# Kernel optimization log

Hardware: AMD Instinct MI355X
Metric: run time of the kernel (lower is better)

## Reference

```python
import jax, jax.numpy as jnp
import numpy as np

IN_CH = 256
OUT_CH = 256
DIM = 8
HEADS = IN_CH // DIM            # 32
TOTAL = HEADS * DIM             # 256
C3 = 3 * TOTAL                  # 768
SCALES = (3, 5)
EPS = 1e-15


def _conv(x, w, b, groups=1, pad=0):
    # x: [B,C,H,W], w: [O, C//groups, kh, kw]
    y = jax.lax.conv_general_dilated(
        x, w, window_strides=(1, 1), padding=[(pad, pad), (pad, pad)],
        dimension_numbers=("NCHW", "OIHW", "NCHW"), feature_group_count=groups)
    return y + b[None, :, None, None]


def setup_inputs() -> dict:
    key = jax.random.key(0)
    ks = jax.random.split(key, 16)
    s = 0.02
    inp = {
        "x": jax.random.normal(ks[0], (8, IN_CH, 64, 64), jnp.float32),
        "qkv_w": jax.random.normal(ks[1], (C3, IN_CH, 1, 1), jnp.float32) * s,
        "qkv_b": jnp.zeros((C3,), jnp.float32),
        # scale 3: depthwise conv (groups=C3) then 1x1 grouped conv (groups=HEADS)
        "dw3_w": jax.random.normal(ks[2], (C3, 1, 3, 3), jnp.float32) * s,
        "dw3_b": jnp.zeros((C3,), jnp.float32),
        "pw3_w": jax.random.normal(ks[3], (C3, C3 // HEADS, 1, 1), jnp.float32) * s,
        "pw3_b": jnp.zeros((C3,), jnp.float32),
        # scale 5
        "dw5_w": jax.random.normal(ks[4], (C3, 1, 5, 5), jnp.float32) * s,
        "dw5_b": jnp.zeros((C3,), jnp.float32),
        "pw5_w": jax.random.normal(ks[5], (C3, C3 // HEADS, 1, 1), jnp.float32) * s,
        "pw5_b": jnp.zeros((C3,), jnp.float32),
        # proj: in = TOTAL*(1+len(SCALES)) = 768 -> OUT_CH
        "proj_w": jax.random.normal(ks[6], (OUT_CH, TOTAL * (1 + len(SCALES)), 1, 1), jnp.float32) * s,
        "proj_b": jnp.zeros((OUT_CH,), jnp.float32),
    }
    return inp


def _relu_linear_att(qkv):
    B, C, H, W = qkv.shape
    qkv = qkv.reshape(B, -1, 3 * DIM, H * W)          # [B, h, 3d, N]
    q = jax.nn.relu(qkv[:, :, :DIM])                   # [B, h, d, N]
    k = jax.nn.relu(qkv[:, :, DIM:2 * DIM])            # [B, h, d, N]
    v = qkv[:, :, 2 * DIM:]                            # [B, h, d, N]
    v = jnp.concatenate([v, jnp.ones_like(v[:, :, :1])], axis=2)  # pad ones -> [B,h,d+1,N]
    vk = jnp.einsum("bhdn,bhen->bhde", v, k)          # [B, h, d+1, d]
    out = jnp.einsum("bhde,bhen->bhdn", vk, q)        # [B, h, d+1, N]
    out = out[:, :, :-1] / (out[:, :, -1:] + EPS)      # normalize by denominator row
    return out.reshape(B, -1, H, W)


def reference(x, qkv_w, qkv_b, dw3_w, dw3_b, pw3_w, pw3_b,
              dw5_w, dw5_b, pw5_w, pw5_b, proj_w, proj_b):
    qkv = _conv(x, qkv_w, qkv_b)                                   # [B, 768, H, W]
    s3 = _conv(_conv(qkv, dw3_w, dw3_b, groups=C3, pad=1), pw3_w, pw3_b, groups=HEADS)
    s5 = _conv(_conv(qkv, dw5_w, dw5_b, groups=C3, pad=2), pw5_w, pw5_b, groups=HEADS)
    multi = jnp.concatenate([qkv, s3, s5], axis=1)                 # [B, 2304, H, W]
    att = _relu_linear_att(multi)                                  # [B, 768, H, W]
    return _conv(att, proj_w, proj_b)                              # [B, 256, H, W]
```

## Files before the change

kernel.cpp:

```cpp
#include <hip/hip_runtime.h>
#include <hip/hip_bf16.h>

#define C3 768
#define PIX 4096
#define NB 8

typedef __attribute__((ext_vector_type(8))) short bf16x8;
typedef __attribute__((ext_vector_type(4))) float f32x4;

__device__ __forceinline__ unsigned short f2bf(float f) {
    unsigned int u = __float_as_uint(f);
    u += 0x7fffu + ((u >> 16) & 1u);
    return (unsigned short)(u >> 16);
}
__device__ __forceinline__ float bf2f(unsigned short h) {
    return __uint_as_float((unsigned int)h << 16);
}

__device__ __forceinline__ void gload_lds16(const void* g, void* l) {
    __builtin_amdgcn_global_load_lds(
        (const __attribute__((address_space(1))) void*)g,
        (__attribute__((address_space(3))) void*)l, 16, 0, 0);
}

__global__ __launch_bounds__(256) void split3_kernel(
    const float* __restrict__ src, unsigned short* __restrict__ d,
    size_t stride, int n)
{
    int i = blockIdx.x * 256 + threadIdx.x;
    if (i < n) {
        float f = src[i];
        unsigned short h0 = f2bf(f);  float r1 = f - bf2f(h0);
        unsigned short h1 = f2bf(r1); float r2 = r1 - bf2f(h1);
        d[i]              = h0;
        d[i + stride]     = h1;
        d[i + 2 * stride] = f2bf(r2);
    }
}

__global__ __launch_bounds__(256) void split2_kernel(
    const float* __restrict__ src, unsigned short* __restrict__ d,
    size_t stride, int n)
{
    int i = blockIdx.x * 256 + threadIdx.x;
    if (i < n) {
        float f = src[i];
        unsigned short h0 = f2bf(f);
        d[i]          = h0;
        d[i + stride] = f2bf(f - bf2f(h0));
    }
}

__global__ __launch_bounds__(256) void transpose_split3_kernel(
    const float* __restrict__ src, unsigned short* __restrict__ d, size_t stride)
{
    __shared__ float t[32][33];
    const int b  = blockIdx.z;
    const int p0 = blockIdx.x * 32;
    const int k0 = blockIdx.y * 32;
    const int tx = threadIdx.x & 31, ty = threadIdx.x >> 5;

    const float* s = src + ((size_t)b * 256 + k0) * PIX + p0;
#pragma unroll
    for (int i = 0; i < 4; ++i)
        t[ty + i * 8][tx] = s[(size_t)(ty + i * 8) * PIX + tx];
    __syncthreads();
#pragma unroll
    for (int i = 0; i < 4; ++i) {
        const int p = ty + i * 8;
        float f = t[tx][p];
        unsigned short h0 = f2bf(f);  float r1 = f - bf2f(h0);
        unsigned short h1 = f2bf(r1); float r2 = r1 - bf2f(h1);
        size_t o = ((size_t)b * PIX + p0 + p) * 256 + k0 + tx;
        d[o]              = h0;
        d[o + stride]     = h1;
        d[o + 2 * stride] = f2bf(r2);
    }
}

template <int K, int S>
__global__ __launch_bounds__(256) void gemm_mfma_splitS(
    const unsigned short* __restrict__ A, const unsigned short* __restrict__ Bm,
    const float* __restrict__ bias, float* __restrict__ Y,
    int Mtiles, int M, size_t strideA, size_t strideB)
{
    __shared__ char lds[S * 24576];
    char* sA[S];
    char* sB[S];
#pragma unroll
    for (int s = 0; s < S; ++s) {
        sA[s] = lds + s * 16384;
        sB[s] = lds + S * 16384 + s * 8192;
    }

    const int nwg = gridDim.x;
    const int per = nwg >> 3;
    const int bid = blockIdx.x;
    const int wg  = (bid & 7) * per + (bid >> 3);
    const int tm  = wg % Mtiles;
    const int tn  = wg / Mtiles;
    const int bm  = tm * 128;
    const int gn0 = tn * 64;

    const int tid  = threadIdx.x;
    const int lane = tid & 63;
    const int wv   = tid >> 6;
    const int m0w  = (wv & 1) * 64;
    const int n0w  = (wv >> 1) * 32;

    const int l8  = lane >> 3;
    const int c16 = (lane & 7) * 16;
    const int gchunk = (c16 ^ (l8 << 4)) >> 1;
    const unsigned short* gA = A  + (size_t)(bm  + wv * 8 + l8) * K + gchunk;
    const unsigned short* gB = Bm + (size_t)(gn0 + wv * 8 + l8) * K + gchunk;
    const int ldsw = wv * 1024;

    f32x4 acc[4][2] = {};

    for (int k0 = 0; k0 < K; k0 += 64) {
        __syncthreads();
#pragma unroll
        for (int s = 0; s < S; ++s) {
#pragma unroll
            for (int j = 0; j < 4; ++j)
                gload_lds16(gA + s * strideA + (size_t)j * 32 * K + k0,
                            sA[s] + ldsw + j * 4096);
#pragma unroll
            for (int j = 0; j < 2; ++j)
                gload_lds16(gB + s * strideB + (size_t)j * 32 * K + k0,
                            sB[s] + ldsw + j * 4096);
        }
        __syncthreads();

#pragma unroll
        for (int kk = 0; kk < 2; ++kk) {
            const int kbyte = (kk * 32 + (lane >> 4) * 8) * 2;
            bf16x8 bfr[S][2];
#pragma unroll
            for (int ni = 0; ni < 2; ++ni) {
                const int r = n0w + ni * 16 + (lane & 15);
                const int byte = r * 128 + (kbyte ^ ((r & 7) << 4));
#pragma unroll
                for (int s = 0; s < S; ++s)
                    bfr[s][ni] = *(const bf16x8*)(sB[s] + byte);
            }
#pragma unroll
            for (int mi = 0; mi < 4; ++mi) {
                bf16x8 afr[S];
                const int r = m0w + mi * 16 + (lane & 15);
                const int byte = r * 128 + (kbyte ^ ((r & 7) << 4));
#pragma unroll
                for (int s = 0; s < S; ++s)
                    afr[s] = *(const bf16x8*)(sA[s] + byte);
#pragma unroll
                for (int ni = 0; ni < 2; ++ni) {
#pragma unroll
                    for (int i = 0; i < S; ++i)
#pragma unroll
                        for (int j = 0; j < S; ++j)
                            if (i + j < S)
                                acc[mi][ni] = __builtin_amdgcn_mfma_f32_16x16x32_bf16(
                                    afr[i], bfr[j][ni], acc[mi][ni], 0, 0, 0);
                }
            }
        }
    }

    const int b  = gn0 >> 12;
    const int p0 = gn0 & 4095;
#pragma unroll
    for (int mi = 0; mi < 4; ++mi)
#pragma unroll
        for (int ni = 0; ni < 2; ++ni) {
            const int p = p0 + n0w + ni * 16 + (lane & 15);
#pragma unroll
            for (int i = 0; i < 4; ++i) {
                const int m = bm + m0w + mi * 16 + (lane >> 4) * 4 + i;
                Y[((size_t)b * M + m) * PIX + p] = acc[mi][ni][i] + bias[m];
            }
        }
}

__global__ __launch_bounds__(256, 4) void dwpw_kernel(
    const float* __restrict__ qkv,
    const float* __restrict__ w3,  const float* __restrict__ b3,
    const float* __restrict__ w5,  const float* __restrict__ b5,
    const float* __restrict__ pw3w, const float* __restrict__ pw3b,
    const float* __restrict__ pw5w, const float* __restrict__ pw5b,
    float* __restrict__ t3, float* __restrict__ t5)
{
    __shared__ float tile[2][8][68];

    const int g   = blockIdx.y;
    const int b   = blockIdx.z;
    const int tid = threadIdx.x;
    const int p   = blockIdx.x * 256 + tid;
    const int r0  = blockIdx.x * 4;
    const int c0  = g * 24;
    const int lr  = tid >> 6;
    const int lc  = tid & 63;

    const float* src0 = qkv + ((size_t)b * C3 + c0) * PIX;

    float o3[24], o5[24];
#pragma unroll
    for (int co = 0; co < 24; ++co) {
        o3[co] = pw3b[c0 + co];
        o5[co] = pw5b[c0 + co];
    }

    auto stage = [&](int ic, int buf) {
        const float* src = src0 + (size_t)ic * PIX;
#pragma unroll
        for (int j = 0; j < 2; ++j) {
            const int rr = (tid >> 6) + j * 4;
            const int cc = tid & 63;
            const int gr = r0 - 2 + rr, gc = cc - 2;
            float v = 0.f;
            if ((unsigned)gr < 64u && (unsigned)gc < 64u) v = src[gr * 64 + gc];
            tile[buf][rr][cc] = v;
        }
        if (tid < 32) {
            const int rr = tid >> 2;
            const int cc = 64 + (tid & 3);
            const int gr = r0 - 2 + rr, gc = cc - 2;
            float v = 0.f;
            if ((unsigned)gr < 64u && (unsigned)gc < 64u) v = src[gr * 64 + gc];
            tile[buf][rr][cc] = v;
        }
    };

    stage(0, 0);
    for (int ic = 0; ic < 24; ++ic) {
        __syncthreads();
        if (ic + 1 < 24) stage(ic + 1, (ic + 1) & 1);

        const int c = c0 + ic;
        const float* k5 = w5 + c * 25;
        const float* k3 = w3 + c * 9;
        const float (*T)[68] = tile[ic & 1];

        float acc3 = b3[c], acc5 = b5[c];
#pragma unroll
        for (int dy = 0; dy < 5; ++dy) {
#pragma unroll
            for (int dx = 0; dx < 5; ++dx) {
                const float v = T[lr + dy][lc + dx];
                acc5 = fmaf(k5[dy * 5 + dx], v, acc5);
                if (dy >= 1 && dy <= 3 && dx >= 1 && dx <= 3)
                    acc3 = fmaf(k3[(dy - 1) * 3 + (dx - 1)], v, acc3);
            }
        }

        const float* w3g = pw3w + (size_t)c0 * 24 + ic;
        const float* w5g = pw5w + (size_t)c0 * 24 + ic;
#pragma unroll
        for (int co = 0; co < 24; ++co) {
            o3[co] = fmaf(w3g[co * 24], acc3, o3[co]);
            o5[co] = fmaf(w5g[co * 24], acc5, o5[co]);
        }
    }

    float* dst3 = t3 + ((size_t)b * C3 + c0) * PIX + p;
    float* dst5 = t5 + ((size_t)b * C3 + c0) * PIX + p;
#pragma unroll
    for (int co = 0; co < 24; ++co) {
        dst3[(size_t)co * PIX] = o3[co];
        dst5[(size_t)co * PIX] = o5[co];
    }
}

__global__ __launch_bounds__(256) void vk_reduce_kernel(
    const float* __restrict__ qkv, const float* __restrict__ s3,
    const float* __restrict__ s5, float* __restrict__ vkout)
{
    const int hh = blockIdx.x;
    const int b  = blockIdx.y;
    const float* src = (hh < 32) ? qkv : ((hh < 64) ? s3 : s5);
    const int ch0 = (hh & 31) * 24;
    const float* base = src + ((size_t)b * C3 + ch0) * PIX;

    float acc[9][8] = {};
    for (int p = threadIdx.x; p < PIX; p += 256) {
        float kk[8], vv[8];
#pragma unroll
        for (int e = 0; e < 8; ++e) kk[e] = fmaxf(base[(8 + e) * PIX + p], 0.f);
#pragma unroll
        for (int d = 0; d < 8; ++d) vv[d] = base[(16 + d) * PIX + p];
#pragma unroll
        for (int d = 0; d < 8; ++d)
#pragma unroll
            for (int e = 0; e < 8; ++e)
                acc[d][e] = fmaf(vv[d], kk[e], acc[d][e]);
#pragma unroll
        for (int e = 0; e < 8; ++e) acc[8][e] += kk[e];
    }

#pragma unroll
    for (int i = 0; i < 9; ++i)
#pragma unroll
        for (int j = 0; j < 8; ++j) {
            float s = acc[i][j];
            for (int off = 32; off; off >>= 1) s += __shfl_down(s, off, 64);
            acc[i][j] = s;
        }

    __shared__ float red[4][72];
    const int wave = threadIdx.x >> 6, lane = threadIdx.x & 63;
    if (lane == 0) {
#pragma unroll
        for (int i = 0; i < 9; ++i)
#pragma unroll
            for (int j = 0; j < 8; ++j) red[wave][i * 8 + j] = acc[i][j];
    }
    __syncthreads();
    const int t = threadIdx.x;
    if (t < 72) {
        float s = red[0][t] + red[1][t] + red[2][t] + red[3][t];
        vkout[((size_t)b * 96 + hh) * 72 + t] = s;
    }
}

__global__ __launch_bounds__(256) void att_apply_kernel(
    const float* __restrict__ qkv, const float* __restrict__ s3,
    const float* __restrict__ s5, const float* __restrict__ vkin,
    unsigned short* __restrict__ aT, size_t stride)
{
    const int hh = blockIdx.y;
    const int b  = blockIdx.z;
    const int p  = blockIdx.x * 256 + threadIdx.x;

    __shared__ float vk[72];
    if (threadIdx.x < 72)
        vk[threadIdx.x] = vkin[((size_t)b * 96 + hh) * 72 + threadIdx.x];
    __syncthreads();

    const float* src = (hh < 32) ? qkv : ((hh < 64) ? s3 : s5);
    const int ch0 = (hh & 31) * 24;
    const float* base = src + ((size_t)b * C3 + ch0) * PIX + p;

    float q[8];
#pragma unroll
    for (int e = 0; e < 8; ++e) q[e] = fmaxf(base[(size_t)e * PIX], 0.f);

    float den = 0.f;
#pragma unroll
    for (int e = 0; e < 8; ++e) den = fmaf(vk[64 + e], q[e], den);
    const float inv = 1.f / (den + 1e-15f);

    union { unsigned short u[8]; uint4 v; } H, L;
#pragma unroll
    for (int d = 0; d < 8; ++d) {
        float num = 0.f;
#pragma unroll
        for (int e = 0; e < 8; ++e) num = fmaf(vk[d * 8 + e], q[e], num);
        float o = num * inv;
        unsigned short h = f2bf(o);
        H.u[d] = h;
        L.u[d] = f2bf(o - bf2f(h));
    }
    const size_t row = (size_t)b * PIX + p;
    *(uint4*)(aT + row * C3 + hh * 8) = H.v;
    *(uint4*)(aT + stride + row * C3 + hh * 8) = L.v;
}

extern "C" void kernel_launch(void* const* d_in, const int* in_sizes, int n_in,
                              void* d_out, int out_size, void* d_ws, size_t ws_size,
                              hipStream_t stream)
{
    const float* x      = (const float*)d_in[0];
    const float* qkv_w  = (const float*)d_in[1];
    const float* qkv_b  = (const float*)d_in[2];
    const float* dw3_w  = (const float*)d_in[3];
    const float* dw3_b  = (const float*)d_in[4];
    const float* pw3_w  = (const float*)d_in[5];
    const float* pw3_b  = (const float*)d_in[6];
    const float* dw5_w  = (const float*)d_in[7];
    const float* dw5_b  = (const float*)d_in[8];
    const float* pw5_w  = (const float*)d_in[9];
    const float* pw5_b  = (const float*)d_in[10];
    const float* proj_w = (const float*)d_in[11];
    const float* proj_b = (const float*)d_in[12];
    float* out = (float*)d_out;

    const size_t SZb = (size_t)C3 * PIX;
    const size_t XTb = (size_t)256 * PIX;
    const int    NW  = C3 * 256;

    const size_t wbytes = (3 + 2) * (size_t)NW * 2;

    int cb = NB;
    while (cb > 1) {
        size_t need = wbytes +
                      (size_t)cb * (3 * SZb * 4 + 3 * XTb * 2 + 2 * SZb * 2 +
                                    (size_t)96 * 72 * 4);
        if (need <= ws_size) break;
        cb >>= 1;
    }

    char* wp = (char*)d_ws;
    unsigned short* WQ = (unsigned short*)wp;   wp += 3 * (size_t)NW * 2;
    unsigned short* WP = (unsigned short*)wp;   wp += 2 * (size_t)NW * 2;
    float* qkv = (float*)wp;                    wp += (size_t)cb * SZb * 4;
    float* t3  = (float*)wp;                    wp += (size_t)cb * SZb * 4;
    float* t5  = (float*)wp;                    wp += (size_t)cb * SZb * 4;
    unsigned short* xT = (unsigned short*)wp;   wp += 3 * (size_t)cb * XTb * 2;
    unsigned short* aT = (unsigned short*)wp;   wp += 2 * (size_t)cb * SZb * 2;
    float* vkb = (float*)wp;

    const size_t strideXT = (size_t)cb * XTb;
    const size_t strideAT = (size_t)cb * SZb;

    split3_kernel<<<(NW + 255) / 256, 256, 0, stream>>>(qkv_w, WQ, (size_t)NW, NW);
    split2_kernel<<<(NW + 255) / 256, 256, 0, stream>>>(proj_w, WP, (size_t)NW, NW);

    for (int b0 = 0; b0 < NB; b0 += cb) {
        const float* xb = x   + (size_t)b0 * 256 * PIX;
        float*       ob = out + (size_t)b0 * 256 * PIX;

        transpose_split3_kernel<<<dim3(128, 8, cb), 256, 0, stream>>>(xb, xT, strideXT);

        gemm_mfma_splitS<256, 3><<<dim3(6 * cb * 64), 256, 0, stream>>>(
            WQ, xT, qkv_b, qkv, 6, C3, (size_t)NW, strideXT);

        dwpw_kernel<<<dim3(16, 32, cb), 256, 0, stream>>>(
            qkv, dw3_w, dw3_b, dw5_w, dw5_b,
            pw3_w, pw3_b, pw5_w, pw5_b, t3, t5);

        vk_reduce_kernel<<<dim3(96, cb), 256, 0, stream>>>(qkv, t3, t5, vkb);

        att_apply_kernel<<<dim3(16, 96, cb), 256, 0, stream>>>(
            qkv, t3, t5, vkb, aT, strideAT);

        gemm_mfma_splitS<768, 2><<<dim3(2 * cb * 64), 256, 0, stream>>>(
            WP, aT, proj_b, ob, 2, 256, (size_t)NW, strideAT);
    }
}
```

Measured before the change: 536.4 us.

## Stage six depthwise channels per barrier in dwpw kernel and raise occupancy hint

The depthwise+pointwise kernel now stages six input channels into shared memory per double-buffered step instead of one. This cuts the number of __syncthreads barriers from 24 to 4 and issues more global loads per stage. The tile row pitch changes to 69 floats and staging uses a linear index split by division and modulo. The launch-bounds minimum blocks per CU goes from 4 to 5. LDS use rises sixfold to about 26 KB per block, which may limit occupancy, and the tighter register budget may cause spills of the 48 accumulators.

```diff
diff --git a/kernel.cpp b/kernel.cpp
--- a/kernel.cpp
+++ b/kernel.cpp
@@ -181,7 +181,7 @@
         }
 }
 
-__global__ __launch_bounds__(256, 4) void dwpw_kernel(
+__global__ __launch_bounds__(256, 5) void dwpw_kernel(
     const float* __restrict__ qkv,
     const float* __restrict__ w3,  const float* __restrict__ b3,
     const float* __restrict__ w5,  const float* __restrict__ b5,
@@ -189,16 +189,15 @@
     const float* __restrict__ pw5w, const float* __restrict__ pw5b,
     float* __restrict__ t3, float* __restrict__ t5)
 {
-    __shared__ float tile[2][8][68];
+    __shared__ float tile[2][6][8][69];
 
     const int g   = blockIdx.y;
     const int b   = blockIdx.z;
     const int tid = threadIdx.x;
-    const int p   = blockIdx.x * 256 + tid;
     const int r0  = blockIdx.x * 4;
-    const int c0  = g * 24;
     const int lr  = tid >> 6;
     const int lc  = tid & 63;
+    const int c0  = g * 24;
 
     const float* src0 = qkv + ((size_t)b * C3 + c0) * PIX;
 
@@ -209,58 +208,66 @@
         o5[co] = pw5b[c0 + co];
     }
 
-    auto stage = [&](int ic, int buf) {
-        const float* src = src0 + (size_t)ic * PIX;
-#pragma unroll
-        for (int j = 0; j < 2; ++j) {
-            const int rr = (tid >> 6) + j * 4;
-            const int cc = tid & 63;
-            const int gr = r0 - 2 + rr, gc = cc - 2;
-            float v = 0.f;
-            if ((unsigned)gr < 64u && (unsigned)gc < 64u) v = src[gr * 64 + gc];
-            tile[buf][rr][cc] = v;
-        }
-        if (tid < 32) {
-            const int rr = tid >> 2;
-            const int cc = 64 + (tid & 3);
-            const int gr = r0 - 2 + rr, gc = cc - 2;
-            float v = 0.f;
-            if ((unsigned)gr < 64u && (unsigned)gc < 64u) v = src[gr * 64 + gc];
-            tile[buf][rr][cc] = v;
+    auto stage = [&](int bt, int buf) {
+#pragma unroll
+        for (int chl = 0; chl < 6; ++chl) {
+            const float* src = src0 + (size_t)(bt * 6 + chl) * PIX;
+#pragma unroll
+            for (int j = 0; j < 2; ++j) {
+                const int e  = j * 256 + tid;
+                const int rr = e / 68, cc = e % 68;
+                const int gr = r0 - 2 + rr, gc = cc - 2;
+                float v = 0.f;
+                if ((unsigned)gr < 64u && (unsigned)gc < 64u) v = src[gr * 64 + gc];
+                tile[buf][chl][rr][cc] = v;
+            }
+            if (tid < 32) {
+                const int e  = 512 + tid;
+                const int rr = e / 68, cc = e % 68;
+                const int gr = r0 - 2 + rr, gc = cc - 2;
+                float v = 0.f;
+                if ((unsigned)gr < 64u && (unsigned)gc < 64u) v = src[gr * 64 + gc];
+                tile[buf][chl][rr][cc] = v;
+            }
         }
     };
 
     stage(0, 0);
-    for (int ic = 0; ic < 24; ++ic) {
+    for (int bt = 0; bt < 4; ++bt) {
         __syncthreads();
-        if (ic + 1 < 24) stage(ic + 1, (ic + 1) & 1);
-
-        const int c = c0 + ic;
-        const float* k5 = w5 + c * 25;
-        const float* k3 = w3 + c * 9;
-        const float (*T)[68] = tile[ic & 1];
-
-        float acc3 = b3[c], acc5 = b5[c];
-#pragma unroll
-        for (int dy = 0; dy < 5; ++dy) {
-#pragma unroll
-            for (int dx = 0; dx < 5; ++dx) {
-                const float v = T[lr + dy][lc + dx];
-                acc5 = fmaf(k5[dy * 5 + dx], v, acc5);
-                if (dy >= 1 && dy <= 3 && dx >= 1 && dx <= 3)
-                    acc3 = fmaf(k3[(dy - 1) * 3 + (dx - 1)], v, acc3);
-            }
-        }
-
-        const float* w3g = pw3w + (size_t)c0 * 24 + ic;
-        const float* w5g = pw5w + (size_t)c0 * 24 + ic;
-#pragma unroll
-        for (int co = 0; co < 24; ++co) {
-            o3[co] = fmaf(w3g[co * 24], acc3, o3[co]);
-            o5[co] = fmaf(w5g[co * 24], acc5, o5[co]);
-        }
-    }
-
+        if (bt + 1 < 4) stage(bt + 1, (bt + 1) & 1);
+
+#pragma unroll
+        for (int chl = 0; chl < 6; ++chl) {
+            const int ic = bt * 6 + chl;
+            const int ch = c0 + ic;
+            const float* k5w = w5 + ch * 25;
+            const float* k3w = w3 + ch * 9;
+            const float (*T)[69] = tile[bt & 1][chl];
+
+            float a3 = b3[ch], a5 = b5[ch];
+#pragma unroll
+            for (int dy = 0; dy < 5; ++dy) {
+#pragma unroll
+                for (int dx = 0; dx < 5; ++dx) {
+                    const float v = T[lr + dy][lc + dx];
+                    a5 = fmaf(k5w[dy * 5 + dx], v, a5);
+                    if (dy >= 1 && dy <= 3 && dx >= 1 && dx <= 3)
+                        a3 = fmaf(k3w[(dy - 1) * 3 + (dx - 1)], v, a3);
+                }
+            }
+
+            const float* w3g = pw3w + (size_t)c0 * 24 + ic;
+            const float* w5g = pw5w + (size_t)c0 * 24 + ic;
+#pragma unroll
+            for (int co = 0; co < 24; ++co) {
+                o3[co] = fmaf(w3g[co * 24], a3, o3[co]);
+                o5[co] = fmaf(w5g[co * 24], a5, o5[co]);
+            }
+        }
+    }
+
+    const int p = (r0 + lr) * 64 + lc;
     float* dst3 = t3 + ((size_t)b * C3 + c0) * PIX + p;
     float* dst5 = t5 + ((size_t)b * C3 + c0) * PIX + p;
 #pragma unroll
```

After: 537.8 us. No clear change (+0.3%).
